# Performance work log

Hardware: AMD Instinct MI355X
Metric: run time of the kernel (lower is better)

The kernel has to match this reference:

```python
import jax, jax.numpy as jnp
import numpy as np

DV = 512   # node feature size
DE = 256   # edge feature size
N = 128    # valid node num (human_nums + obj_nums)
B = 8
K = 3      # propagate_layers
C = 117    # hoi_classes


def gru_cell(x, h, w_ih, w_hh, b_ih, b_hh):
    # PyTorch nn.GRU single step, gate order (r, z, n)
    gi = w_ih @ x + b_ih
    gh = w_hh @ h + b_hh
    ir, iz, inn = jnp.split(gi, 3)
    hr, hz, hn = jnp.split(gh, 3)
    r = jax.nn.sigmoid(ir + hr)
    z = jax.nn.sigmoid(iz + hz)
    n = jnp.tanh(inn + r * hn)
    return (1.0 - z) * n + z * h


def _run_graph(h, e, w_link, b_link, w_msg, b_msg, w_ih, w_hh, b_ih, b_hh):
    # h: [dv, N], e: [de, N, N]
    wl_j = w_link[:DV]          # applied to Feature[:dv, i, :] = h (column index j)
    wl_i = w_link[DV:2 * DV]    # applied to Feature[dv:2dv, :, i] = h (row index i)
    wl_e = w_link[2 * DV:]
    adj = jnp.zeros((N, N), h.dtype)
    for _ in range(K):
        # link function on Feature built under torch.no_grad -> stop_gradient
        hs = jax.lax.stop_gradient(h)
        es = jax.lax.stop_gradient(e)
        logits = (wl_i @ hs)[:, None] + (wl_j @ hs)[None, :] \
                 + jnp.einsum('c,cij->ij', wl_e, es) + b_link
        adj = jax.nn.sigmoid(logits)  # [N, N]

        def node_step(carry, i):
            h, e = carry
            h_v = h[:, i]                      # [dv]
            e_row = e[:, i, :]                 # [de, N] (rows < i already updated this round)
            comb = jnp.concatenate(
                [jnp.broadcast_to(h_v[:, None], (DV, N)), h, e_row], axis=0)  # [2dv+de, N]
            m = jax.nn.relu(w_msg @ comb + b_msg[:, None])                    # [de, N]
            e = e.at[:, i, :].set(m)
            m_sum = (m * adj[i][None, :]).sum(axis=1)                         # [de]
            h_new = gru_cell(m_sum, h_v, w_ih, w_hh, b_ih, b_hh)
            h = h.at[:, i].set(h_new)
            return (h, e), None

        (h, e), _ = jax.lax.scan(node_step, (h, e), jnp.arange(N))
    return adj, h


def setup_inputs() -> dict:
    key = jax.random.key(0)
    ks = jax.random.split(key, 8)
    s = 0.02
    return {
        "edge_features": jax.random.normal(ks[0], (B, N, N, DE), jnp.float32),
        "node_features": jax.random.normal(ks[1], (B, N, DV), jnp.float32),
        "adj_mat": jnp.zeros((B, N, N), jnp.float32),
        "node_labels": jnp.zeros((B, N, C), jnp.float32),
        "human_nums": jnp.full((B,), 32, jnp.int32),
        "obj_nums": jnp.full((B,), 96, jnp.int32),
        "w_link": jax.random.normal(ks[2], (2 * DV + DE,), jnp.float32) * s,
        "b_link": jnp.zeros((), jnp.float32),
        "w_msg": jax.random.normal(ks[3], (DE, 2 * DV + DE), jnp.float32) * s,
        "b_msg": jnp.zeros((DE,), jnp.float32),
        "w_ih": jax.random.normal(ks[4], (3 * DV, DE), jnp.float32) * s,
        "w_hh": jax.random.normal(ks[5], (3 * DV, DV), jnp.float32) * s,
        "b_ih": jnp.zeros((3 * DV,), jnp.float32),
        "b_hh": jnp.zeros((3 * DV,), jnp.float32),
        "w_ro": jax.random.normal(ks[6], (C, DV), jnp.float32) * s,
        "b_ro": jnp.zeros((C,), jnp.float32),
    }


def reference(edge_features, node_features, adj_mat, node_labels, human_nums,
              obj_nums, w_link, b_link, w_msg, b_msg, w_ih, w_hh, b_ih, b_hh,
              w_ro, b_ro):
    e0 = jnp.transpose(edge_features, (0, 3, 1, 2))  # [B, de, N, N]
    h0 = jnp.transpose(node_features, (0, 2, 1))     # [B, dv, N]
    run = jax.vmap(_run_graph, in_axes=(0, 0) + (None,) * 8)
    pred_adj_mat, h = run(h0, e0, w_link, b_link, w_msg, b_msg,
                          w_ih, w_hh, b_ih, b_hh)
    # readout on the final (post-last-update) node states
    pred_node_labels = jnp.einsum('cd,bdn->bnc', w_ro, h) + b_ro
    return pred_adj_mat, pred_node_labels
```

## Files before the change

kernel.cpp:

```cpp
#include <hip/hip_runtime.h>
#include <math.h>


#define NB 8
#define NN 128
#define DVV 512
#define DEE 256
#define NCC 117
#define SB 16
#define GISLOT 12288

typedef __attribute__((ext_vector_type(8))) short short8;
typedef __attribute__((ext_vector_type(4))) float f32x4;

__device__ __forceinline__ float sigmf(float x) {
  x = fminf(fmaxf(x, -30.f), 30.f);
  return 1.0f / (1.0f + __expf(-x));
}
__device__ __forceinline__ float tanhf_fast(float x) {
  x = fminf(fmaxf(x, -15.f), 15.f);
  float e = __expf(2.0f * x);
  return (e - 1.0f) / (e + 1.0f);
}
__device__ __forceinline__ unsigned short f2bf(float f) {
  union { float f; unsigned u; } v; v.f = f;
  unsigned u = v.u + 0x7FFFu + ((v.u >> 16) & 1u);
  return (unsigned short)(u >> 16);
}
__device__ __forceinline__ float bfu(unsigned short u) {
  union { unsigned u; float f; } v; v.u = ((unsigned)u) << 16; return v.f;
}

__global__ __launch_bounds__(256) void k_copy(const float* __restrict__ src, float* __restrict__ dst,
                                              unsigned short* __restrict__ hb) {
  int i = blockIdx.x * 256 + threadIdx.x;
  float4 v = ((const float4*)src)[i];
  ((float4*)dst)[i] = v;
  unsigned long long pk = (unsigned long long)f2bf(v.x) | ((unsigned long long)f2bf(v.y) << 16)
                        | ((unsigned long long)f2bf(v.z) << 32) | ((unsigned long long)f2bf(v.w) << 48);
  *(unsigned long long*)&hb[i * 4] = pk;
}

__global__ __launch_bounds__(256) void k_cvtw(const float* __restrict__ w_msg,
                                              unsigned short* __restrict__ w3b) {
  int idx = blockIdx.x * 256 + threadIdx.x;
  int r = idx >> 8, c = idx & 255;
  w3b[idx] = f2bf(w_msg[(size_t)r * 1280 + 1024 + c]);
}

__global__ __launch_bounds__(128) void k_av(const float* __restrict__ h, const float* __restrict__ w_link,
                                            float* __restrict__ av) {
  int b = blockIdx.x >> 7, n = blockIdx.x & 127;
  int lane = threadIdx.x & 63, half = threadIdx.x >> 6;
  const float* hc = h + (size_t)((b << 7) + n) * DVV;
  const float* w = w_link + half * DVV;
  float acc = 0.f;
#pragma unroll
  for (int t = 0; t < 8; ++t) { int d = lane + (t << 6); acc += w[d] * hc[d]; }
#pragma unroll
  for (int off = 32; off; off >>= 1) acc += __shfl_down(acc, off);
  if (lane == 0) av[(b << 8) + half * NN + n] = acc;
}

template <int FIRST>
__global__ __launch_bounds__(256) void k_plogit_mfma(
    const float* edge, const unsigned short* eP16in, const unsigned short* __restrict__ w3b,
    const float* __restrict__ w_link, const float* __restrict__ av,
    const float* __restrict__ b_link, unsigned short* eP16out, float* __restrict__ adj_out) {
  int b = blockIdx.x >> 7, i = blockIdx.x & 127;
  __shared__ unsigned short eL[128 * 264];
  int tid = threadIdx.x;

  if (FIRST) {
    const float* s0 = edge + (size_t)(b * NN + i) * NN * DEE;
    for (int l = tid; l < 4096; l += 256) {
      int j = l >> 5, c0 = (l & 31) * 8;
      float4 v0 = *(const float4*)&s0[(size_t)j * DEE + c0];
      float4 v1 = *(const float4*)&s0[(size_t)j * DEE + c0 + 4];
      unsigned long long p0 = (unsigned long long)f2bf(v0.x) | ((unsigned long long)f2bf(v0.y) << 16)
                            | ((unsigned long long)f2bf(v0.z) << 32) | ((unsigned long long)f2bf(v0.w) << 48);
      unsigned long long p1 = (unsigned long long)f2bf(v1.x) | ((unsigned long long)f2bf(v1.y) << 16)
                            | ((unsigned long long)f2bf(v1.z) << 32) | ((unsigned long long)f2bf(v1.w) << 48);
      *(unsigned long long*)&eL[j * 264 + c0] = p0;
      *(unsigned long long*)&eL[j * 264 + c0 + 4] = p1;
    }
  } else {
    const unsigned short* s0 = eP16in + (size_t)(b * NN + i) * DEE * NN;
#pragma unroll
    for (int t = 0; t < 2; ++t) {
      int blk = tid + t * 256;
      int c0 = (blk >> 4) * 8, j0 = (blk & 15) * 8;
      short8 rows[8];
#pragma unroll
      for (int cc = 0; cc < 8; ++cc)
        rows[cc] = *(const short8*)&s0[(size_t)(c0 + cc) * NN + j0];
#pragma unroll
      for (int jj = 0; jj < 8; ++jj) {
        short8 o;
#pragma unroll
        for (int cc = 0; cc < 8; ++cc) o[cc] = rows[cc][jj];
        *(short8*)&eL[(j0 + jj) * 264 + c0] = o;
      }
    }
  }
  __syncthreads();

  float accLE = 0.f;
  if (tid < NN) {
    const unsigned short* row = &eL[tid * 264];
    for (int c = 0; c < DEE; ++c) accLE += w_link[1024 + c] * bfu(row[c]);
  }

  const int w = tid >> 6, l = tid & 63;
  const int lm = l & 15, lg = l >> 4;
  f32x4 acc[4][8];
#pragma unroll
  for (int a = 0; a < 4; ++a)
#pragma unroll
    for (int jt = 0; jt < 8; ++jt) acc[a][jt] = (f32x4){0.f, 0.f, 0.f, 0.f};

#pragma unroll
  for (int kk = 0; kk < 8; ++kk) {
    short8 afr[4];
#pragma unroll
    for (int a = 0; a < 4; ++a)
      afr[a] = *(const short8*)&w3b[(size_t)(64 * w + 16 * a + lm) * 256 + 32 * kk + 8 * lg];
#pragma unroll
    for (int jt = 0; jt < 8; ++jt) {
      short8 bfr = *(const short8*)&eL[(16 * jt + lm) * 264 + 32 * kk + 8 * lg];
#pragma unroll
      for (int a = 0; a < 4; ++a)
        acc[a][jt] = __builtin_amdgcn_mfma_f32_16x16x32_bf16(afr[a], bfr, acc[a][jt], 0, 0, 0);
    }
  }

  unsigned short* Pout = eP16out + (size_t)(b * NN + i) * DEE * NN;
#pragma unroll
  for (int a = 0; a < 4; ++a) {
    int rbase = 64 * w + 16 * a + 4 * lg;
#pragma unroll
    for (int jt = 0; jt < 8; ++jt) {
      int j = 16 * jt + lm;
#pragma unroll
      for (int q = 0; q < 4; ++q)
        Pout[(size_t)(rbase + q) * NN + j] = f2bf(acc[a][jt][q]);
    }
  }
  if (tid < NN) {
    float x = av[(b << 8) + NN + i] + av[(b << 8) + tid] + accLE + b_link[0];
    adj_out[((size_t)b * NN + i) * NN + tid] = sigmf(x);
  }
}

__global__ __launch_bounds__(256) void k_wh3(const float* __restrict__ w_hh, const float* __restrict__ w_msg,
                                             const float* __restrict__ b_hh, const float* __restrict__ b_msg,
                                             const float* __restrict__ h, float* __restrict__ GHo,
                                             float* __restrict__ Uo, float* __restrict__ Go) {
  int bx = blockIdx.x, b = blockIdx.y;
  const float* W; const float* bias; float* out; int ldw, R, r0;
  if (bx < 96)       { W = w_hh;        ldw = 512;  R = 1536; bias = b_hh;   out = GHo; r0 = bx * 16; }
  else if (bx < 112) { W = w_msg;       ldw = 1280; R = 256;  bias = b_msg;  out = Uo;  r0 = (bx - 96) * 16; }
  else               { W = w_msg + 512; ldw = 1280; R = 256;  bias = nullptr; out = Go; r0 = (bx - 112) * 16; }
  __shared__ float hT[128][129];
  __shared__ float wT[16][129];
  __shared__ float outT[16][129];
  int tid = threadIdx.x;
  int n = tid & 127, rr = tid >> 7;
  float acc8[8] = {0, 0, 0, 0, 0, 0, 0, 0};
  for (int dc = 0; dc < DVV; dc += 128) {
    if (dc) __syncthreads();
    for (int l = tid * 4; l < 16384; l += 1024) {
      int nn = l >> 7, d = l & 127;
      float4 v = *(const float4*)&h[((size_t)(b << 7) + nn) * DVV + dc + d];
      hT[d + 0][nn] = v.x; hT[d + 1][nn] = v.y; hT[d + 2][nn] = v.z; hT[d + 3][nn] = v.w;
    }
    for (int l = tid; l < 2048; l += 256) {
      int r = l >> 7, d = l & 127;
      wT[r][d] = W[(size_t)(r0 + r) * ldw + dc + d];
    }
    __syncthreads();
    for (int d = 0; d < 128; ++d) {
      float hval = hT[d][n];
#pragma unroll
      for (int r8 = 0; r8 < 8; ++r8) acc8[r8] += wT[rr * 8 + r8][d] * hval;
    }
  }
#pragma unroll
  for (int r8 = 0; r8 < 8; ++r8) {
    int r = rr * 8 + r8;
    outT[r][n] = acc8[r8] + (bias ? bias[r0 + r] : 0.0f);
  }
  __syncthreads();
  int n2 = tid >> 1, q = tid & 1;
  size_t base = ((size_t)(b << 7) + n2) * R + r0 + q * 8;
  float4 o0; o0.x = outT[q * 8 + 0][n2]; o0.y = outT[q * 8 + 1][n2]; o0.z = outT[q * 8 + 2][n2]; o0.w = outT[q * 8 + 3][n2];
  float4 o1; o1.x = outT[q * 8 + 4][n2]; o1.y = outT[q * 8 + 5][n2]; o1.z = outT[q * 8 + 6][n2]; o1.w = outT[q * 8 + 7][n2];
  *(float4*)&out[base] = o0;
  *(float4*)&out[base + 4] = o1;
}

template <int WRITE_E>
__global__ __launch_bounds__(256) void k_scan13(
    unsigned short* eP16, const float* __restrict__ adj, const float* __restrict__ GH,
    const float* __restrict__ U, const float* __restrict__ Gini, float* __restrict__ h,
    unsigned short* __restrict__ hb, const float* __restrict__ w_ih,
    const float* __restrict__ b_ih, const float* __restrict__ w_msg,
    float* __restrict__ gi, unsigned* __restrict__ flags, int kround) {
  const int s = blockIdx.x, b = blockIdx.y, tid = threadIdx.x;
  __shared__ float wihL[16 * 1540];
  __shared__ __align__(16) float w2L[16 * 520];
  __shared__ __align__(16) float GL[16 * 132];
  __shared__ float hnL[DVV];
  __shared__ float msL[16];

  for (int l = tid; l < 1536 * 16; l += 256) {
    int r = l >> 4, c = l & 15;
    wihL[c * 1540 + r] = w_ih[(size_t)r * 256 + 16 * s + c];
  }
  for (int l = tid; l < 16 * 128; l += 256) {
    int c = l >> 7, d4 = (l & 127) * 4;
    *(float4*)&w2L[c * 520 + d4] = *(const float4*)&w_msg[(size_t)(16 * s + c) * 1280 + 512 + d4];
  }
  for (int l = tid; l < 2048; l += 256) {
    int c = l & 15, j = l >> 4;
    GL[c * 132 + j] = Gini[((size_t)b * NN + j) * DEE + 16 * s + c];
  }
  float bi0 = b_ih[tid], bi1 = b_ih[tid + 256];
  float bi2 = b_ih[512 + tid], bi3 = b_ih[768 + tid];
  float bi4 = b_ih[1024 + tid], bi5 = b_ih[1280 + tid];

  const int c_loc = tid >> 4, jg = tid & 15, j0 = jg << 3;

  short8 Pv; float4 A0, A1; float uu;
  float hv0, hv1, ghr0, ghr1, ghz0, ghz1, ghn0, ghn1;
  {
    size_t rE = ((size_t)(b * NN + 0) * DEE + 16 * s + c_loc) * NN + j0;
    Pv = *(const short8*)&eP16[rE];
    size_t rA = (size_t)(b * NN + 0) * NN + j0;
    A0 = *(const float4*)&adj[rA]; A1 = *(const float4*)&adj[rA + 4];
    uu = U[(size_t)(b * NN + 0) * DEE + 16 * s + c_loc];
    size_t rH = (size_t)(b * NN + 0) * DVV;
    hv0 = h[rH + tid]; hv1 = h[rH + tid + 256];
    size_t rG = (size_t)(b * NN + 0) * 1536;
    ghr0 = GH[rG + tid]; ghr1 = GH[rG + tid + 256];
    ghz0 = GH[rG + 512 + tid]; ghz1 = GH[rG + 768 + tid];
    ghn0 = GH[rG + 1024 + tid]; ghn1 = GH[rG + 1280 + tid];
  }

  for (int i = 0; i < NN; ++i) {
    int g = kround * NN + i;
    float* giA = gi + (size_t)(g % 3) * GISLOT + (size_t)b * 1536;
    float* giZ = gi + (size_t)((g + 1) % 3) * GISLOT + (size_t)b * 1536;
    __syncthreads();

    float acc;
    {
      const float* gl = &GL[c_loc * 132 + j0];
      float4 g0 = *(const float4*)&gl[0];
      float4 g1 = *(const float4*)&gl[4];
      float m0 = fmaxf(uu + g0.x + bfu((unsigned short)Pv[0]), 0.f);
      float m1 = fmaxf(uu + g0.y + bfu((unsigned short)Pv[1]), 0.f);
      float m2 = fmaxf(uu + g0.z + bfu((unsigned short)Pv[2]), 0.f);
      float m3 = fmaxf(uu + g0.w + bfu((unsigned short)Pv[3]), 0.f);
      float m4 = fmaxf(uu + g1.x + bfu((unsigned short)Pv[4]), 0.f);
      float m5 = fmaxf(uu + g1.y + bfu((unsigned short)Pv[5]), 0.f);
      float m6 = fmaxf(uu + g1.z + bfu((unsigned short)Pv[6]), 0.f);
      float m7 = fmaxf(uu + g1.w + bfu((unsigned short)Pv[7]), 0.f);
      acc = A0.x * m0 + A0.y * m1 + A0.z * m2 + A0.w * m3
          + A1.x * m4 + A1.y * m5 + A1.z * m6 + A1.w * m7;
      if (WRITE_E) {
        size_t rE = ((size_t)(b * NN + i) * DEE + 16 * s + c_loc) * NN + j0;
        short8 mw;
        mw[0] = (short)f2bf(m0); mw[1] = (short)f2bf(m1); mw[2] = (short)f2bf(m2); mw[3] = (short)f2bf(m3);
        mw[4] = (short)f2bf(m4); mw[5] = (short)f2bf(m5); mw[6] = (short)f2bf(m6); mw[7] = (short)f2bf(m7);
        *(short8*)&eP16[rE] = mw;
      }
    }
    {
      int in = (i < NN - 1) ? i + 1 : NN - 1;
      size_t rE = ((size_t)(b * NN + in) * DEE + 16 * s + c_loc) * NN + j0;
      Pv = *(const short8*)&eP16[rE];
      size_t rA = (size_t)(b * NN + in) * NN + j0;
      A0 = *(const float4*)&adj[rA]; A1 = *(const float4*)&adj[rA + 4];
      uu = U[(size_t)(b * NN + in) * DEE + 16 * s + c_loc];
    }
    acc += __shfl_down(acc, 8);
    acc += __shfl_down(acc, 4);
    acc += __shfl_down(acc, 2);
    acc += __shfl_down(acc, 1);
    if (jg == 0) msL[c_loc] = acc;
    __syncthreads();

    {
      float ms[16];
#pragma unroll
      for (int c = 0; c < 16; ++c) ms[c] = msL[c];
#pragma unroll
      for (int u = 0; u < 6; ++u) {
        int r = tid + (u << 8);
        float pa = 0.f;
#pragma unroll
        for (int c = 0; c < 16; ++c) pa += wihL[c * 1540 + r] * ms[c];
        (void)__hip_atomic_fetch_add(&giA[r], pa, __ATOMIC_RELAXED, __HIP_MEMORY_SCOPE_SYSTEM);
      }
      if (tid < 96)
        __hip_atomic_store(&giZ[96 * s + tid], 0.f, __ATOMIC_RELAXED, __HIP_MEMORY_SCOPE_SYSTEM);
    }

    {
      unsigned tgt = (unsigned)(g + 1);
      __syncthreads();
      if (tid < 64) {
        if (tid == 0)
          __hip_atomic_store(&flags[(((b << 4) + s) << 5)], tgt, __ATOMIC_RELAXED,
                             __HIP_MEMORY_SCOPE_SYSTEM);
        unsigned* fp = &flags[(((b << 4) + (tid & 15)) << 5)];
        for (;;) {
          unsigned v = __hip_atomic_load(fp, __ATOMIC_RELAXED, __HIP_MEMORY_SCOPE_SYSTEM);
          if (!__any(v < tgt)) break;
          __builtin_amdgcn_s_sleep(1);
        }
      }
      __syncthreads();
    }

    {
      float sr0 = bi0 + __hip_atomic_load(&giA[tid],        __ATOMIC_RELAXED, __HIP_MEMORY_SCOPE_SYSTEM);
      float sr1 = bi1 + __hip_atomic_load(&giA[tid + 256],  __ATOMIC_RELAXED, __HIP_MEMORY_SCOPE_SYSTEM);
      float sz0 = bi2 + __hip_atomic_load(&giA[512 + tid],  __ATOMIC_RELAXED, __HIP_MEMORY_SCOPE_SYSTEM);
      float sz1 = bi3 + __hip_atomic_load(&giA[768 + tid],  __ATOMIC_RELAXED, __HIP_MEMORY_SCOPE_SYSTEM);
      float sn0 = bi4 + __hip_atomic_load(&giA[1024 + tid], __ATOMIC_RELAXED, __HIP_MEMORY_SCOPE_SYSTEM);
      float sn1 = bi5 + __hip_atomic_load(&giA[1280 + tid], __ATOMIC_RELAXED, __HIP_MEMORY_SCOPE_SYSTEM);
      float rg0 = sigmf(sr0 + ghr0), rg1 = sigmf(sr1 + ghr1);
      float z0 = sigmf(sz0 + ghz0),  z1 = sigmf(sz1 + ghz1);
      float nv0 = tanhf_fast(sn0 + rg0 * ghn0);
      float nv1 = tanhf_fast(sn1 + rg1 * ghn1);
      float hn0 = (1.f - z0) * nv0 + z0 * hv0;
      float hn1 = (1.f - z1) * nv1 + z1 * hv1;
      hnL[tid] = hn0; hnL[tid + 256] = hn1;
      size_t rH = (size_t)(b * NN + i) * DVV;
      if ((tid >> 5) == s)         { h[rH + tid] = hn0;       hb[rH + tid] = f2bf(hn0); }
      if (((tid + 256) >> 5) == s) { h[rH + tid + 256] = hn1; hb[rH + tid + 256] = f2bf(hn1); }
    }
    {
      int in = (i < NN - 1) ? i + 1 : NN - 1;
      size_t rH = (size_t)(b * NN + in) * DVV;
      hv0 = h[rH + tid]; hv1 = h[rH + tid + 256];
      size_t rG = (size_t)(b * NN + in) * 1536;
      ghr0 = GH[rG + tid]; ghr1 = GH[rG + tid + 256];
      ghz0 = GH[rG + 512 + tid]; ghz1 = GH[rG + 768 + tid];
      ghn0 = GH[rG + 1024 + tid]; ghn1 = GH[rG + 1280 + tid];
    }
    __syncthreads();

    {
      int cw = tid >> 4, dg = tid & 15;
      float acc2 = 0.f;
#pragma unroll
      for (int it = 0; it < 32; ++it) {
        int d = dg + (it << 4);
        acc2 += w2L[cw * 520 + d] * hnL[d];
      }
      acc2 += __shfl_down(acc2, 8);
      acc2 += __shfl_down(acc2, 4);
      acc2 += __shfl_down(acc2, 2);
      acc2 += __shfl_down(acc2, 1);
      if (dg == 0) GL[cw * 132 + i] = acc2;
    }
  }
}

__global__ __launch_bounds__(128) void k_labels(const float* __restrict__ h, const float* __restrict__ w_ro,
                                                const float* __restrict__ b_ro, float* __restrict__ out) {
  int b = blockIdx.x >> 7, n = blockIdx.x & 127;
  __shared__ __align__(16) float hr[512];
  int tid = threadIdx.x;
  *(float4*)&hr[tid * 4] = *(const float4*)&h[(size_t)((b << 7) + n) * DVV + tid * 4];
  __syncthreads();
  if (tid < NCC) {
    const float* w = w_ro + (size_t)tid * DVV;
    float acc = b_ro[tid];
    for (int d = 0; d < DVV; d += 4) {
      float4 wv = *(const float4*)&w[d];
      acc += wv.x * hr[d] + wv.y * hr[d + 1] + wv.z * hr[d + 2] + wv.w * hr[d + 3];
    }
    out[(size_t)((b << 7) + n) * NCC + tid] = acc;
  }
}

extern "C" void kernel_launch(void* const* d_in, const int* in_sizes, int n_in,
                              void* d_out, int out_size, void* d_ws, size_t ws_size,
                              hipStream_t stream) {
  const float* edge   = (const float*)d_in[0];
  const float* node   = (const float*)d_in[1];
  const float* w_link = (const float*)d_in[6];
  const float* b_link = (const float*)d_in[7];
  const float* w_msg  = (const float*)d_in[8];
  const float* b_msg  = (const float*)d_in[9];
  const float* w_ih   = (const float*)d_in[10];
  const float* w_hh   = (const float*)d_in[11];
  const float* b_ih   = (const float*)d_in[12];
  const float* b_hh   = (const float*)d_in[13];
  const float* w_ro   = (const float*)d_in[14];
  const float* b_ro   = (const float*)d_in[15];
  float* out = (float*)d_out;
  float* ws  = (float*)d_ws;

  unsigned short* eP16 = (unsigned short*)ws;
  unsigned short* hb   = (unsigned short*)(ws + 21000000);
  float* h_buf  = ws + 33554432ull;
  float* GH_buf = h_buf + 524288;
  float* U_buf  = GH_buf + 1572864;
  float* G_buf  = U_buf + 262144;
  float* lE_buf = G_buf + 262144;
  float* av_buf = lE_buf + 131072;
  float* gi_buf = av_buf + 2048;
  unsigned* flags = (unsigned*)(gi_buf + 3 * GISLOT);
  unsigned short* w3b = (unsigned short*)lE_buf;
  size_t need_bytes = 36710304ull * 4ull;
  if (ws_size < need_bytes) return;

  hipMemsetAsync(gi_buf, 0, (3 * GISLOT + 4096) * sizeof(float), stream);
  k_copy<<<512, 256, 0, stream>>>(node, h_buf, hb);
  k_cvtw<<<256, 256, 0, stream>>>(w_msg, w3b);

  for (int k = 0; k < 3; ++k) {
    k_av<<<1024, 128, 0, stream>>>(h_buf, w_link, av_buf);
    if (k == 0) k_plogit_mfma<1><<<1024, 256, 0, stream>>>(edge, eP16, w3b, w_link, av_buf, b_link, eP16, out);
    else        k_plogit_mfma<0><<<1024, 256, 0, stream>>>(edge, eP16, w3b, w_link, av_buf, b_link, eP16, out);
    k_wh3<<<dim3(128, 8), 256, 0, stream>>>(w_hh, w_msg, b_hh, b_msg, h_buf, GH_buf, U_buf, G_buf);
    if (k < 2) k_scan13<1><<<dim3(SB, NB), 256, 0, stream>>>(eP16, out, GH_buf, U_buf, G_buf, h_buf, hb,
                                                             w_ih, b_ih, w_msg, gi_buf, flags, k);
    else       k_scan13<0><<<dim3(SB, NB), 256, 0, stream>>>(eP16, out, GH_buf, U_buf, G_buf, h_buf, hb,
                                                             w_ih, b_ih, w_msg, gi_buf, flags, k);
  }
  k_labels<<<1024, 128, 0, stream>>>(h_buf, w_ro, b_ro, out + 131072);
}
```

Before: 1.953 ms.

## Process two batches per scan block and prefetch next-step loads before flag wait

The sequential scan kernel now handles two graphs per workgroup, halving the grid to 16x4. Each block reuses its shared w_ih and w_msg slices for both batches and interleaves the two independent recurrences, so per-step latency is spread over twice the work. The loads for the next step (edge row, adj, U, h, GH) are issued between publishing the flag and spinning on it, hiding their latency behind the cross-block barrier. The cost is more registers and shared memory per block, fewer concurrent blocks, and roughly twice the serial work per step in each block.

```diff
diff --git a/kernel.cpp b/kernel.cpp
--- a/kernel.cpp
+++ b/kernel.cpp
@@ -200,18 +200,22 @@
 }
 
 template <int WRITE_E>
-__global__ __launch_bounds__(256) void k_scan13(
+__global__ __launch_bounds__(256) void k_scan15(
     unsigned short* eP16, const float* __restrict__ adj, const float* __restrict__ GH,
     const float* __restrict__ U, const float* __restrict__ Gini, float* __restrict__ h,
     unsigned short* __restrict__ hb, const float* __restrict__ w_ih,
     const float* __restrict__ b_ih, const float* __restrict__ w_msg,
     float* __restrict__ gi, unsigned* __restrict__ flags, int kround) {
-  const int s = blockIdx.x, b = blockIdx.y, tid = threadIdx.x;
+  const int s = blockIdx.x, bg = blockIdx.y, tid = threadIdx.x;
+  const int b0 = 2 * bg, b1 = 2 * bg + 1;
   __shared__ float wihL[16 * 1540];
   __shared__ __align__(16) float w2L[16 * 520];
-  __shared__ __align__(16) float GL[16 * 132];
-  __shared__ float hnL[DVV];
-  __shared__ float msL[16];
+  __shared__ __align__(16) float GL0[16 * 132];
+  __shared__ __align__(16) float GL1[16 * 132];
+  __shared__ float hnL0[DVV];
+  __shared__ float hnL1[DVV];
+  __shared__ float msL0[16];
+  __shared__ float msL1[16];
 
   for (int l = tid; l < 1536 * 16; l += 256) {
     int r = l >> 4, c = l & 15;
@@ -223,7 +227,8 @@
   }
   for (int l = tid; l < 2048; l += 256) {
     int c = l & 15, j = l >> 4;
-    GL[c * 132 + j] = Gini[((size_t)b * NN + j) * DEE + 16 * s + c];
+    GL0[c * 132 + j] = Gini[((size_t)b0 * NN + j) * DEE + 16 * s + c];
+    GL1[c * 132 + j] = Gini[((size_t)b1 * NN + j) * DEE + 16 * s + c];
   }
   float bi0 = b_ih[tid], bi1 = b_ih[tid + 256];
   float bi2 = b_ih[512 + tid], bi3 = b_ih[768 + tid];
@@ -231,45 +236,59 @@
 
   const int c_loc = tid >> 4, jg = tid & 15, j0 = jg << 3;
 
-  short8 Pv; float4 A0, A1; float uu;
-  float hv0, hv1, ghr0, ghr1, ghz0, ghz1, ghn0, ghn1;
+  short8 Pv0, Pv1; float4 A00, A01, A10, A11; float uu0, uu1;
+  float hv00, hv01, ghr00, ghr01, ghz00, ghz01, ghn00, ghn01;
+  float hv10, hv11, ghr10, ghr11, ghz10, ghz11, ghn10, ghn11;
   {
-    size_t rE = ((size_t)(b * NN + 0) * DEE + 16 * s + c_loc) * NN + j0;
-    Pv = *(const short8*)&eP16[rE];
-    size_t rA = (size_t)(b * NN + 0) * NN + j0;
-    A0 = *(const float4*)&adj[rA]; A1 = *(const float4*)&adj[rA + 4];
-    uu = U[(size_t)(b * NN + 0) * DEE + 16 * s + c_loc];
-    size_t rH = (size_t)(b * NN + 0) * DVV;
-    hv0 = h[rH + tid]; hv1 = h[rH + tid + 256];
-    size_t rG = (size_t)(b * NN + 0) * 1536;
-    ghr0 = GH[rG + tid]; ghr1 = GH[rG + tid + 256];
-    ghz0 = GH[rG + 512 + tid]; ghz1 = GH[rG + 768 + tid];
-    ghn0 = GH[rG + 1024 + tid]; ghn1 = GH[rG + 1280 + tid];
+    size_t rE = ((size_t)(b0 * NN + 0) * DEE + 16 * s + c_loc) * NN + j0;
+    Pv0 = *(const short8*)&eP16[rE];
+    size_t rA = (size_t)(b0 * NN + 0) * NN + j0;
+    A00 = *(const float4*)&adj[rA]; A01 = *(const float4*)&adj[rA + 4];
+    uu0 = U[(size_t)(b0 * NN + 0) * DEE + 16 * s + c_loc];
+    size_t rH = (size_t)(b0 * NN + 0) * DVV;
+    hv00 = h[rH + tid]; hv01 = h[rH + tid + 256];
+    size_t rG = (size_t)(b0 * NN + 0) * 1536;
+    ghr00 = GH[rG + tid]; ghr01 = GH[rG + tid + 256];
+    ghz00 = GH[rG + 512 + tid]; ghz01 = GH[rG + 768 + tid];
+    ghn00 = GH[rG + 1024 + tid]; ghn01 = GH[rG + 1280 + tid];
+    rE = ((size_t)(b1 * NN + 0) * DEE + 16 * s + c_loc) * NN + j0;
+    Pv1 = *(const short8*)&eP16[rE];
+    rA = (size_t)(b1 * NN + 0) * NN + j0;
+    A10 = *(const float4*)&adj[rA]; A11 = *(const float4*)&adj[rA + 4];
+    uu1 = U[(size_t)(b1 * NN + 0) * DEE + 16 * s + c_loc];
+    rH = (size_t)(b1 * NN + 0) * DVV;
+    hv10 = h[rH + tid]; hv11 = h[rH + tid + 256];
+    rG = (size_t)(b1 * NN + 0) * 1536;
+    ghr10 = GH[rG + tid]; ghr11 = GH[rG + tid + 256];
+    ghz10 = GH[rG + 512 + tid]; ghz11 = GH[rG + 768 + tid];
+    ghn10 = GH[rG + 1024 + tid]; ghn11 = GH[rG + 1280 + tid];
   }
 
   for (int i = 0; i < NN; ++i) {
     int g = kround * NN + i;
-    float* giA = gi + (size_t)(g % 3) * GISLOT + (size_t)b * 1536;
-    float* giZ = gi + (size_t)((g + 1) % 3) * GISLOT + (size_t)b * 1536;
+    float* giA0 = gi + (size_t)(g % 3) * GISLOT + (size_t)b0 * 1536;
+    float* giZ0 = gi + (size_t)((g + 1) % 3) * GISLOT + (size_t)b0 * 1536;
+    float* giA1 = gi + (size_t)(g % 3) * GISLOT + (size_t)b1 * 1536;
+    float* giZ1 = gi + (size_t)((g + 1) % 3) * GISLOT + (size_t)b1 * 1536;
     __syncthreads();
 
-    float acc;
+    float acc0, acc1;
     {
-      const float* gl = &GL[c_loc * 132 + j0];
+      const float* gl = &GL0[c_loc * 132 + j0];
       float4 g0 = *(const float4*)&gl[0];
       float4 g1 = *(const float4*)&gl[4];
-      float m0 = fmaxf(uu + g0.x + bfu((unsigned short)Pv[0]), 0.f);
-      float m1 = fmaxf(uu + g0.y + bfu((unsigned short)Pv[1]), 0.f);
-      float m2 = fmaxf(uu + g0.z + bfu((unsigned short)Pv[2]), 0.f);
-      float m3 = fmaxf(uu + g0.w + bfu((unsigned short)Pv[3]), 0.f);
-      float m4 = fmaxf(uu + g1.x + bfu((unsigned short)Pv[4]), 0.f);
-      float m5 = fmaxf(uu + g1.y + bfu((unsigned short)Pv[5]), 0.f);
-      float m6 = fmaxf(uu + g1.z + bfu((unsigned short)Pv[6]), 0.f);
-      float m7 = fmaxf(uu + g1.w + bfu((unsigned short)Pv[7]), 0.f);
-      acc = A0.x * m0 + A0.y * m1 + A0.z * m2 + A0.w * m3
-          + A1.x * m4 + A1.y * m5 + A1.z * m6 + A1.w * m7;
+      float m0 = fmaxf(uu0 + g0.x + bfu((unsigned short)Pv0[0]), 0.f);
+      float m1 = fmaxf(uu0 + g0.y + bfu((unsigned short)Pv0[1]), 0.f);
+      float m2 = fmaxf(uu0 + g0.z + bfu((unsigned short)Pv0[2]), 0.f);
+      float m3 = fmaxf(uu0 + g0.w + bfu((unsigned short)Pv0[3]), 0.f);
+      float m4 = fmaxf(uu0 + g1.x + bfu((unsigned short)Pv0[4]), 0.f);
+      float m5 = fmaxf(uu0 + g1.y + bfu((unsigned short)Pv0[5]), 0.f);
+      float m6 = fmaxf(uu0 + g1.z + bfu((unsigned short)Pv0[6]), 0.f);
+      float m7 = fmaxf(uu0 + g1.w + bfu((unsigned short)Pv0[7]), 0.f);
+      acc0 = A00.x * m0 + A00.y * m1 + A00.z * m2 + A00.w * m3
+           + A01.x * m4 + A01.y * m5 + A01.z * m6 + A01.w * m7;
       if (WRITE_E) {
-        size_t rE = ((size_t)(b * NN + i) * DEE + 16 * s + c_loc) * NN + j0;
+        size_t rE = ((size_t)(b0 * NN + i) * DEE + 16 * s + c_loc) * NN + j0;
         short8 mw;
         mw[0] = (short)f2bf(m0); mw[1] = (short)f2bf(m1); mw[2] = (short)f2bf(m2); mw[3] = (short)f2bf(m3);
         mw[4] = (short)f2bf(m4); mw[5] = (short)f2bf(m5); mw[6] = (short)f2bf(m6); mw[7] = (short)f2bf(m7);
@@ -277,95 +296,157 @@
       }
     }
     {
-      int in = (i < NN - 1) ? i + 1 : NN - 1;
-      size_t rE = ((size_t)(b * NN + in) * DEE + 16 * s + c_loc) * NN + j0;
-      Pv = *(const short8*)&eP16[rE];
-      size_t rA = (size_t)(b * NN + in) * NN + j0;
-      A0 = *(const float4*)&adj[rA]; A1 = *(const float4*)&adj[rA + 4];
-      uu = U[(size_t)(b * NN + in) * DEE + 16 * s + c_loc];
-    }
-    acc += __shfl_down(acc, 8);
-    acc += __shfl_down(acc, 4);
-    acc += __shfl_down(acc, 2);
-    acc += __shfl_down(acc, 1);
-    if (jg == 0) msL[c_loc] = acc;
+      const float* gl = &GL1[c_loc * 132 + j0];
+      float4 g0 = *(const float4*)&gl[0];
+      float4 g1 = *(const float4*)&gl[4];
+      float m0 = fmaxf(uu1 + g0.x + bfu((unsigned short)Pv1[0]), 0.f);
+      float m1 = fmaxf(uu1 + g0.y + bfu((unsigned short)Pv1[1]), 0.f);
+      float m2 = fmaxf(uu1 + g0.z + bfu((unsigned short)Pv1[2]), 0.f);
+      float m3 = fmaxf(uu1 + g0.w + bfu((unsigned short)Pv1[3]), 0.f);
+      float m4 = fmaxf(uu1 + g1.x + bfu((unsigned short)Pv1[4]), 0.f);
+      float m5 = fmaxf(uu1 + g1.y + bfu((unsigned short)Pv1[5]), 0.f);
+      float m6 = fmaxf(uu1 + g1.z + bfu((unsigned short)Pv1[6]), 0.f);
+      float m7 = fmaxf(uu1 + g1.w + bfu((unsigned short)Pv1[7]), 0.f);
+      acc1 = A10.x * m0 + A10.y * m1 + A10.z * m2 + A10.w * m3
+           + A11.x * m4 + A11.y * m5 + A11.z * m6 + A11.w * m7;
+      if (WRITE_E) {
+        size_t rE = ((size_t)(b1 * NN + i) * DEE + 16 * s + c_loc) * NN + j0;
+        short8 mw;
+        mw[0] = (short)f2bf(m0); mw[1] = (short)f2bf(m1); mw[2] = (short)f2bf(m2); mw[3] = (short)f2bf(m3);
+        mw[4] = (short)f2bf(m4); mw[5] = (short)f2bf(m5); mw[6] = (short)f2bf(m6); mw[7] = (short)f2bf(m7);
+        *(short8*)&eP16[rE] = mw;
+      }
+    }
+    acc0 += __shfl_down(acc0, 8); acc1 += __shfl_down(acc1, 8);
+    acc0 += __shfl_down(acc0, 4); acc1 += __shfl_down(acc1, 4);
+    acc0 += __shfl_down(acc0, 2); acc1 += __shfl_down(acc1, 2);
+    acc0 += __shfl_down(acc0, 1); acc1 += __shfl_down(acc1, 1);
+    if (jg == 0) { msL0[c_loc] = acc0; msL1[c_loc] = acc1; }
     __syncthreads();
 
     {
-      float ms[16];
-#pragma unroll
-      for (int c = 0; c < 16; ++c) ms[c] = msL[c];
+      float ms0[16], ms1[16];
+#pragma unroll
+      for (int c = 0; c < 16; ++c) { ms0[c] = msL0[c]; ms1[c] = msL1[c]; }
 #pragma unroll
       for (int u = 0; u < 6; ++u) {
         int r = tid + (u << 8);
-        float pa = 0.f;
-#pragma unroll
-        for (int c = 0; c < 16; ++c) pa += wihL[c * 1540 + r] * ms[c];
-        (void)__hip_atomic_fetch_add(&giA[r], pa, __ATOMIC_RELAXED, __HIP_MEMORY_SCOPE_SYSTEM);
-      }
-      if (tid < 96)
-        __hip_atomic_store(&giZ[96 * s + tid], 0.f, __ATOMIC_RELAXED, __HIP_MEMORY_SCOPE_SYSTEM);
-    }
-
-    {
-      unsigned tgt = (unsigned)(g + 1);
-      __syncthreads();
-      if (tid < 64) {
-        if (tid == 0)
-          __hip_atomic_store(&flags[(((b << 4) + s) << 5)], tgt, __ATOMIC_RELAXED,
-                             __HIP_MEMORY_SCOPE_SYSTEM);
-        unsigned* fp = &flags[(((b << 4) + (tid & 15)) << 5)];
-        for (;;) {
-          unsigned v = __hip_atomic_load(fp, __ATOMIC_RELAXED, __HIP_MEMORY_SCOPE_SYSTEM);
-          if (!__any(v < tgt)) break;
-          __builtin_amdgcn_s_sleep(1);
+        float pa0 = 0.f, pa1 = 0.f;
+#pragma unroll
+        for (int c = 0; c < 16; ++c) {
+          float wv = wihL[c * 1540 + r];
+          pa0 += wv * ms0[c]; pa1 += wv * ms1[c];
         }
-      }
-      __syncthreads();
-    }
-
-    {
-      float sr0 = bi0 + __hip_atomic_load(&giA[tid],        __ATOMIC_RELAXED, __HIP_MEMORY_SCOPE_SYSTEM);
-      float sr1 = bi1 + __hip_atomic_load(&giA[tid + 256],  __ATOMIC_RELAXED, __HIP_MEMORY_SCOPE_SYSTEM);
-      float sz0 = bi2 + __hip_atomic_load(&giA[512 + tid],  __ATOMIC_RELAXED, __HIP_MEMORY_SCOPE_SYSTEM);
-      float sz1 = bi3 + __hip_atomic_load(&giA[768 + tid],  __ATOMIC_RELAXED, __HIP_MEMORY_SCOPE_SYSTEM);
-      float sn0 = bi4 + __hip_atomic_load(&giA[1024 + tid], __ATOMIC_RELAXED, __HIP_MEMORY_SCOPE_SYSTEM);
-      float sn1 = bi5 + __hip_atomic_load(&giA[1280 + tid], __ATOMIC_RELAXED, __HIP_MEMORY_SCOPE_SYSTEM);
-      float rg0 = sigmf(sr0 + ghr0), rg1 = sigmf(sr1 + ghr1);
-      float z0 = sigmf(sz0 + ghz0),  z1 = sigmf(sz1 + ghz1);
-      float nv0 = tanhf_fast(sn0 + rg0 * ghn0);
-      float nv1 = tanhf_fast(sn1 + rg1 * ghn1);
-      float hn0 = (1.f - z0) * nv0 + z0 * hv0;
-      float hn1 = (1.f - z1) * nv1 + z1 * hv1;
-      hnL[tid] = hn0; hnL[tid + 256] = hn1;
-      size_t rH = (size_t)(b * NN + i) * DVV;
-      if ((tid >> 5) == s)         { h[rH + tid] = hn0;       hb[rH + tid] = f2bf(hn0); }
-      if (((tid + 256) >> 5) == s) { h[rH + tid + 256] = hn1; hb[rH + tid + 256] = f2bf(hn1); }
-    }
+        (void)__hip_atomic_fetch_add(&giA0[r], pa0, __ATOMIC_RELAXED, __HIP_MEMORY_SCOPE_SYSTEM);
+        (void)__hip_atomic_fetch_add(&giA1[r], pa1, __ATOMIC_RELAXED, __HIP_MEMORY_SCOPE_SYSTEM);
+      }
+      if (tid < 96) {
+        __hip_atomic_store(&giZ0[96 * s + tid], 0.f, __ATOMIC_RELAXED, __HIP_MEMORY_SCOPE_SYSTEM);
+        __hip_atomic_store(&giZ1[96 * s + tid], 0.f, __ATOMIC_RELAXED, __HIP_MEMORY_SCOPE_SYSTEM);
+      }
+    }
+
+    unsigned tgt = (unsigned)(g + 1);
+    __syncthreads();
+    if (tid == 0)
+      __hip_atomic_store(&flags[(((bg << 4) + s) << 5)], tgt, __ATOMIC_RELAXED,
+                         __HIP_MEMORY_SCOPE_SYSTEM);
+    float t_hv00, t_hv01, t_ghr00, t_ghr01, t_ghz00, t_ghz01, t_ghn00, t_ghn01;
+    float t_hv10, t_hv11, t_ghr10, t_ghr11, t_ghz10, t_ghz11, t_ghn10, t_ghn11;
     {
       int in = (i < NN - 1) ? i + 1 : NN - 1;
-      size_t rH = (size_t)(b * NN + in) * DVV;
-      hv0 = h[rH + tid]; hv1 = h[rH + tid + 256];
-      size_t rG = (size_t)(b * NN + in) * 1536;
-      ghr0 = GH[rG + tid]; ghr1 = GH[rG + tid + 256];
-      ghz0 = GH[rG + 512 + tid]; ghz1 = GH[rG + 768 + tid];
-      ghn0 = GH[rG + 1024 + tid]; ghn1 = GH[rG + 1280 + tid];
-    }
+      size_t rE = ((size_t)(b0 * NN + in) * DEE + 16 * s + c_loc) * NN + j0;
+      Pv0 = *(const short8*)&eP16[rE];
+      size_t rA = (size_t)(b0 * NN + in) * NN + j0;
+      A00 = *(const float4*)&adj[rA]; A01 = *(const float4*)&adj[rA + 4];
+      uu0 = U[(size_t)(b0 * NN + in) * DEE + 16 * s + c_loc];
+      size_t rH = (size_t)(b0 * NN + in) * DVV;
+      t_hv00 = h[rH + tid]; t_hv01 = h[rH + tid + 256];
+      size_t rG = (size_t)(b0 * NN + in) * 1536;
+      t_ghr00 = GH[rG + tid]; t_ghr01 = GH[rG + tid + 256];
+      t_ghz00 = GH[rG + 512 + tid]; t_ghz01 = GH[rG + 768 + tid];
+      t_ghn00 = GH[rG + 1024 + tid]; t_ghn01 = GH[rG + 1280 + tid];
+      rE = ((size_t)(b1 * NN + in) * DEE + 16 * s + c_loc) * NN + j0;
+      Pv1 = *(const short8*)&eP16[rE];
+      rA = (size_t)(b1 * NN + in) * NN + j0;
+      A10 = *(const float4*)&adj[rA]; A11 = *(const float4*)&adj[rA + 4];
+      uu1 = U[(size_t)(b1 * NN + in) * DEE + 16 * s + c_loc];
+      rH = (size_t)(b1 * NN + in) * DVV;
+      t_hv10 = h[rH + tid]; t_hv11 = h[rH + tid + 256];
+      rG = (size_t)(b1 * NN + in) * 1536;
+      t_ghr10 = GH[rG + tid]; t_ghr11 = GH[rG + tid + 256];
+      t_ghz10 = GH[rG + 512 + tid]; t_ghz11 = GH[rG + 768 + tid];
+      t_ghn10 = GH[rG + 1024 + tid]; t_ghn11 = GH[rG + 1280 + tid];
+    }
+    if (tid < 64) {
+      unsigned* fp = &flags[(((bg << 4) + (tid & 15)) << 5)];
+      for (;;) {
+        unsigned v = __hip_atomic_load(fp, __ATOMIC_RELAXED, __HIP_MEMORY_SCOPE_SYSTEM);
+        if (!__any(v < tgt)) break;
+        __builtin_amdgcn_s_sleep(1);
+      }
+    }
+    __syncthreads();
+
+    {
+      float q00 = __hip_atomic_load(&giA0[tid],        __ATOMIC_RELAXED, __HIP_MEMORY_SCOPE_SYSTEM);
+      float q01 = __hip_atomic_load(&giA0[tid + 256],  __ATOMIC_RELAXED, __HIP_MEMORY_SCOPE_SYSTEM);
+      float q02 = __hip_atomic_load(&giA0[512 + tid],  __ATOMIC_RELAXED, __HIP_MEMORY_SCOPE_SYSTEM);
+      float q03 = __hip_atomic_load(&giA0[768 + tid],  __ATOMIC_RELAXED, __HIP_MEMORY_SCOPE_SYSTEM);
+      float q04 = __hip_atomic_load(&giA0[1024 + tid], __ATOMIC_RELAXED, __HIP_MEMORY_SCOPE_SYSTEM);
+      float q05 = __hip_atomic_load(&giA0[1280 + tid], __ATOMIC_RELAXED, __HIP_MEMORY_SCOPE_SYSTEM);
+      float q10 = __hip_atomic_load(&giA1[tid],        __ATOMIC_RELAXED, __HIP_MEMORY_SCOPE_SYSTEM);
+      float q11 = __hip_atomic_load(&giA1[tid + 256],  __ATOMIC_RELAXED, __HIP_MEMORY_SCOPE_SYSTEM);
+      float q12 = __hip_atomic_load(&giA1[512 + tid],  __ATOMIC_RELAXED, __HIP_MEMORY_SCOPE_SYSTEM);
+      float q13 = __hip_atomic_load(&giA1[768 + tid],  __ATOMIC_RELAXED, __HIP_MEMORY_SCOPE_SYSTEM);
+      float q14 = __hip_atomic_load(&giA1[1024 + tid], __ATOMIC_RELAXED, __HIP_MEMORY_SCOPE_SYSTEM);
+      float q15 = __hip_atomic_load(&giA1[1280 + tid], __ATOMIC_RELAXED, __HIP_MEMORY_SCOPE_SYSTEM);
+      {
+        float rg0 = sigmf(bi0 + q00 + ghr00), rg1 = sigmf(bi1 + q01 + ghr01);
+        float z0 = sigmf(bi2 + q02 + ghz00),  z1 = sigmf(bi3 + q03 + ghz01);
+        float nv0 = tanhf_fast(bi4 + q04 + rg0 * ghn00);
+        float nv1 = tanhf_fast(bi5 + q05 + rg1 * ghn01);
+        float hn0 = (1.f - z0) * nv0 + z0 * hv00;
+        float hn1 = (1.f - z1) * nv1 + z1 * hv01;
+        hnL0[tid] = hn0; hnL0[tid + 256] = hn1;
+        size_t rH = (size_t)(b0 * NN + i) * DVV;
+        if ((tid >> 5) == s)         { h[rH + tid] = hn0;       hb[rH + tid] = f2bf(hn0); }
+        if (((tid + 256) >> 5) == s) { h[rH + tid + 256] = hn1; hb[rH + tid + 256] = f2bf(hn1); }
+      }
+      {
+        float rg0 = sigmf(bi0 + q10 + ghr10), rg1 = sigmf(bi1 + q11 + ghr11);
+        float z0 = sigmf(bi2 + q12 + ghz10),  z1 = sigmf(bi3 + q13 + ghz11);
+        float nv0 = tanhf_fast(bi4 + q14 + rg0 * ghn10);
+        float nv1 = tanhf_fast(bi5 + q15 + rg1 * ghn11);
+        float hn0 = (1.f - z0) * nv0 + z0 * hv10;
+        float hn1 = (1.f - z1) * nv1 + z1 * hv11;
+        hnL1[tid] = hn0; hnL1[tid + 256] = hn1;
+        size_t rH = (size_t)(b1 * NN + i) * DVV;
+        if ((tid >> 5) == s)         { h[rH + tid] = hn0;       hb[rH + tid] = f2bf(hn0); }
+        if (((tid + 256) >> 5) == s) { h[rH + tid + 256] = hn1; hb[rH + tid + 256] = f2bf(hn1); }
+      }
+    }
+    hv00 = t_hv00; hv01 = t_hv01; ghr00 = t_ghr00; ghr01 = t_ghr01;
+    ghz00 = t_ghz00; ghz01 = t_ghz01; ghn00 = t_ghn00; ghn01 = t_ghn01;
+    hv10 = t_hv10; hv11 = t_hv11; ghr10 = t_ghr10; ghr11 = t_ghr11;
+    ghz10 = t_ghz10; ghz11 = t_ghz11; ghn10 = t_ghn10; ghn11 = t_ghn11;
     __syncthreads();
 
     {
       int cw = tid >> 4, dg = tid & 15;
-      float acc2 = 0.f;
+      float a0 = 0.f, a1 = 0.f;
 #pragma unroll
       for (int it = 0; it < 32; ++it) {
         int d = dg + (it << 4);
-        acc2 += w2L[cw * 520 + d] * hnL[d];
-      }
-      acc2 += __shfl_down(acc2, 8);
-      acc2 += __shfl_down(acc2, 4);
-      acc2 += __shfl_down(acc2, 2);
-      acc2 += __shfl_down(acc2, 1);
-      if (dg == 0) GL[cw * 132 + i] = acc2;
+        float wv = w2L[cw * 520 + d];
+        a0 += wv * hnL0[d];
+        a1 += wv * hnL1[d];
+      }
+      a0 += __shfl_down(a0, 8); a1 += __shfl_down(a1, 8);
+      a0 += __shfl_down(a0, 4); a1 += __shfl_down(a1, 4);
+      a0 += __shfl_down(a0, 2); a1 += __shfl_down(a1, 2);
+      a0 += __shfl_down(a0, 1); a1 += __shfl_down(a1, 1);
+      if (dg == 0) { GL0[cw * 132 + i] = a0; GL1[cw * 132 + i] = a1; }
     }
   }
 }
@@ -429,10 +510,10 @@
     if (k == 0) k_plogit_mfma<1><<<1024, 256, 0, stream>>>(edge, eP16, w3b, w_link, av_buf, b_link, eP16, out);
     else        k_plogit_mfma<0><<<1024, 256, 0, stream>>>(edge, eP16, w3b, w_link, av_buf, b_link, eP16, out);
     k_wh3<<<dim3(128, 8), 256, 0, stream>>>(w_hh, w_msg, b_hh, b_msg, h_buf, GH_buf, U_buf, G_buf);
-    if (k < 2) k_scan13<1><<<dim3(SB, NB), 256, 0, stream>>>(eP16, out, GH_buf, U_buf, G_buf, h_buf, hb,
-                                                             w_ih, b_ih, w_msg, gi_buf, flags, k);
-    else       k_scan13<0><<<dim3(SB, NB), 256, 0, stream>>>(eP16, out, GH_buf, U_buf, G_buf, h_buf, hb,
-                                                             w_ih, b_ih, w_msg, gi_buf, flags, k);
+    if (k < 2) k_scan15<1><<<dim3(SB, NB / 2), 256, 0, stream>>>(eP16, out, GH_buf, U_buf, G_buf, h_buf, hb,
+                                                                 w_ih, b_ih, w_msg, gi_buf, flags, k);
+    else       k_scan15<0><<<dim3(SB, NB / 2), 256, 0, stream>>>(eP16, out, GH_buf, U_buf, G_buf, h_buf, hb,
+                                                                 w_ih, b_ih, w_msg, gi_buf, flags, k);
   }
   k_labels<<<1024, 128, 0, stream>>>(h_buf, w_ro, b_ro, out + 131072);
 }
```

After: 2.187 ms. 12.0% more time.
